# Performance work log

Hardware: AMD Instinct MI355X
Metric: run time of the kernel (lower is better)

The kernel has to match this reference:

```python
import jax, jax.numpy as jnp
import numpy as np

B, NX, NY, H = 512, 128, 128, 512


def setup_inputs() -> dict:
    key = jax.random.key(0)
    ks = jax.random.split(key, 8)
    s1 = 1.0 / np.sqrt(NX + NY)
    s2 = 1.0 / np.sqrt(H)
    return {
        "x": jax.random.normal(ks[0], (B, NX), dtype=jnp.float32),
        "y": jax.random.normal(ks[1], (B, NY), dtype=jnp.float32),
        "W1": jax.random.normal(ks[2], (H, NX + NY), dtype=jnp.float32) * s1,
        "b1": jax.random.normal(ks[3], (H,), dtype=jnp.float32) * s1,
        "W2": jax.random.normal(ks[4], (H, H), dtype=jnp.float32) * s2,
        "b2": jax.random.normal(ks[5], (H,), dtype=jnp.float32) * s2,
        "W3": jax.random.normal(ks[6], (1, H), dtype=jnp.float32) * s2,
        "b3": jax.random.normal(ks[7], (1,), dtype=jnp.float32) * s2,
    }


def reference(x, y, W1, b1, W2, b2, W3, b3):
    # Torch semantics: pair_input row k = concat(x[k % B], y[k // B]),
    # so scores.view(B,B)[i, j] = mlp(concat(x[j], y[i])).
    Nx = x.shape[1]
    hx = jnp.einsum('jn,hn->jh', x, W1[:, :Nx])          # [B_x, H]
    hy = jnp.einsum('in,hn->ih', y, W1[:, Nx:])          # [B_y, H]
    h1 = jax.nn.relu(hy[:, None, :] + hx[None, :, :] + b1)   # [B_y, B_x, H]
    h2 = jax.nn.relu(jnp.einsum('ijh,gh->ijg', h1, W2) + b2)  # [B_y, B_x, H]
    scores = jnp.einsum('ijh,oh->ijo', h2, W3) + b3          # [B_y, B_x, 1]
    return (scores[..., 0], 0.0)
```

## Files before the change

### kernel.cpp

```cpp
#include <hip/hip_runtime.h>

#define B_ 512
#define H_ 512

typedef short short8 __attribute__((ext_vector_type(8)));
typedef float f32x4 __attribute__((ext_vector_type(4)));

__device__ __forceinline__ unsigned short bf16rne(float f) {
  unsigned u = __float_as_uint(f);
  u += 0x7FFFu + ((u >> 16) & 1u);
  return (unsigned short)(u >> 16);
}

__global__ __launch_bounds__(256) void k_pre(const float* __restrict__ x,
                                             const float* __restrict__ y,
                                             const float* __restrict__ W1,
                                             const float* __restrict__ b1,
                                             const float* __restrict__ W2,
                                             float* __restrict__ hx,
                                             float* __restrict__ hy,
                                             unsigned short* __restrict__ w2p) {
  __shared__ float xs[4][128];
  const int blk = blockIdx.x;
  const int t = threadIdx.x;
  if (blk < 256) {
    const bool isx = blk < 128;
    const int r0 = (isx ? blk : blk - 128) * 4;
    const float* src = (isx ? x : y) + r0 * 128;
    if (t < 128) ((float4*)xs)[t] = ((const float4*)src)[t];
    __syncthreads();
    const int woff = isx ? 0 : 128;
    float* dst = (isx ? hx : hy) + r0 * H_;
#pragma unroll
    for (int hh = 0; hh < 2; ++hh) {
      const int h = t + hh * 256;
      const float4* wr = (const float4*)(W1 + h * 256 + woff);
      float a0 = isx ? b1[h] : 0.f, a1 = a0, a2 = a0, a3 = a0;
#pragma unroll
      for (int n = 0; n < 32; ++n) {
        float4 w = wr[n];
        float4 v0 = ((const float4*)xs[0])[n];
        float4 v1 = ((const float4*)xs[1])[n];
        float4 v2 = ((const float4*)xs[2])[n];
        float4 v3 = ((const float4*)xs[3])[n];
        a0 = fmaf(w.x, v0.x, fmaf(w.y, v0.y, fmaf(w.z, v0.z, fmaf(w.w, v0.w, a0))));
        a1 = fmaf(w.x, v1.x, fmaf(w.y, v1.y, fmaf(w.z, v1.z, fmaf(w.w, v1.w, a1))));
        a2 = fmaf(w.x, v2.x, fmaf(w.y, v2.y, fmaf(w.z, v2.z, fmaf(w.w, v2.w, a2))));
        a3 = fmaf(w.x, v3.x, fmaf(w.y, v3.y, fmaf(w.z, v3.z, fmaf(w.w, v3.w, a3))));
      }
      dst[h] = a0;
      dst[H_ + h] = a1;
      dst[2 * H_ + h] = a2;
      dst[3 * H_ + h] = a3;
    }
  } else {
    int d = (blk - 256) * 256 + t;
    int e = d & 7;
    int g15 = (d >> 3) & 15;
    int ks = (d >> 7) & 3;
    int nf = (d >> 9) & 7;
    int plane = (d >> 12) & 1;
    int c = (d >> 13) & 15;
    int nt = (d >> 17) & 3;
    int g = nt * 128 + nf * 16 + g15;
    int k = c * 32 + ks * 8 + e;
    float v = W2[g * H_ + k];
    unsigned short h = bf16rne(v);
    float r = v - __uint_as_float(((unsigned)h) << 16);
    w2p[d] = plane ? bf16rne(r) : h;
  }
}

__device__ __forceinline__ unsigned chop2(float x0, float x1, float y0,
                                          float y1) {
  float t0 = fmaxf(x0 + y0, 0.f);
  float t1 = fmaxf(x1 + y1, 0.f);
  return __builtin_amdgcn_perm(__float_as_uint(t1), __float_as_uint(t0),
                               0x07060302);
}

union Frag { unsigned u[4]; short8 s; };

#define BUILD_FRAG(NXT, m_)                                                   \
  {                                                                           \
    NXT[m_].u[0] = chop2(X0.x, X0.y, Ya[m_].x, Ya[m_].y);                     \
    NXT[m_].u[1] = chop2(X0.z, X0.w, Ya[m_].z, Ya[m_].w);                     \
    NXT[m_].u[2] = chop2(X1.x, X1.y, Yb[m_].x, Yb[m_].y);                     \
    NXT[m_].u[3] = chop2(X1.z, X1.w, Yb[m_].z, Yb[m_].w);                     \
  }

#define CHUNK_STEP(c_, buf_, CUR, NXT)                                        \
  {                                                                           \
    if ((c_) < 15) STAGE((c_) + 1, (buf_) ^ 1);                               \
    const int ko_ = ((c_) + 1) * 32;                                          \
    X0 = *(const float4*)(hxp + ko_);                                         \
    X1 = *(const float4*)(hxp + ko_ + 4);                                     \
    _Pragma("unroll") for (int m = 0; m < 4; ++m) {                           \
      Ya[m] = *(const float4*)(hyp + m * H_ + ko_);                           \
      Yb[m] = *(const float4*)(hyp + m * H_ + ko_ + 4);                       \
    }                                                                         \
    const unsigned short* bb_ = (buf_) ? bbr1 : bbr0;                         \
    _Pragma("unroll") for (int nf = 0; nf < 8; ++nf) {                        \
      short8 Bh = *(const short8*)(bb_ + nf * 512);                           \
      short8 Bl = *(const short8*)(bb_ + 4096 + nf * 512);                    \
      __builtin_amdgcn_s_setprio(1);                                          \
      _Pragma("unroll") for (int m = 0; m < 4; ++m) {                         \
        f32x4 a = acc[m][nf];                                                 \
        a = __builtin_amdgcn_mfma_f32_16x16x32_bf16(CUR[m].s, Bl, a, 0, 0, 0);\
        a = __builtin_amdgcn_mfma_f32_16x16x32_bf16(CUR[m].s, Bh, a, 0, 0, 0);\
        acc[m][nf] = a;                                                       \
      }                                                                       \
      __builtin_amdgcn_s_setprio(0);                                          \
      if ((nf) >= 4) BUILD_FRAG(NXT, (nf) - 4);                               \
    }                                                                         \
    __syncthreads();                                                          \
  }

__global__ __launch_bounds__(256, 2) void k_main(
    const float* __restrict__ hx, const float* __restrict__ hy,
    const unsigned short* __restrict__ w2p,
    const float* __restrict__ b2, const float* __restrict__ w3,
    const float* __restrict__ b3, float* __restrict__ out) {
  __shared__ alignas(16) unsigned short Bs[2][8192];

  const int tid = threadIdx.x;
  const int lane = tid & 63;
  const int wid = tid >> 6;

  const int bid = blockIdx.x;
  const int ntile = bid & 3;
  const int mtile = bid >> 2;
  const int ibase = (mtile >> 5) << 4;
  const int jbase = (mtile & 31) << 4;
  const int l15 = lane & 15;
  const int kslot = (lane >> 4) << 3;

  const float* hxp = hx + (jbase + l15) * H_ + kslot;
  const float* hyp = hy + (ibase + wid * 4) * H_ + kslot;

  const unsigned short* gstage = w2p + ntile * 131072 + wid * 2048 + lane * 8;
  unsigned short* lds_dst0 = &Bs[0][wid * 2048];
  unsigned short* lds_dst1 = &Bs[1][wid * 2048];
  const unsigned short* bbr0 = &Bs[0][0] + lane * 8;
  const unsigned short* bbr1 = &Bs[1][0] + lane * 8;

  auto STAGE = [&](int c, int buf) {
    const unsigned short* g = gstage + c * 8192;
    unsigned short* l = buf ? lds_dst1 : lds_dst0;
#pragma unroll
    for (int q = 0; q < 4; ++q) {
      __builtin_amdgcn_global_load_lds(
          (const __attribute__((address_space(1))) unsigned int*)(g + q * 512),
          (__attribute__((address_space(3))) unsigned int*)(l + q * 512),
          16, 0, 0);
    }
  };

  f32x4 acc[4][8] = {};
  Frag F[4], G[4];
  float4 X0, X1, Ya[4], Yb[4];

  STAGE(0, 0);
  X0 = *(const float4*)(hxp);
  X1 = *(const float4*)(hxp + 4);
#pragma unroll
  for (int m = 0; m < 4; ++m) {
    Ya[m] = *(const float4*)(hyp + m * H_);
    Yb[m] = *(const float4*)(hyp + m * H_ + 4);
  }
#pragma unroll
  for (int m = 0; m < 4; ++m) BUILD_FRAG(F, m);
  __syncthreads();

  for (int cc = 0; cc < 8; ++cc) {
    CHUNK_STEP(2 * cc, 0, F, G);
    CHUNK_STEP(2 * cc + 1, 1, G, F);
  }

  const int gbase = ntile << 7;
  float b2v[8], w3v[8];
#pragma unroll
  for (int nf = 0; nf < 8; ++nf) {
    int g = gbase + nf * 16 + l15;
    b2v[nf] = b2[g];
    w3v[nf] = w3[g];
  }
  const float b3v = (ntile == 0) ? b3[0] : 0.f;
#pragma unroll
  for (int mf = 0; mf < 4; ++mf) {
#pragma unroll
    for (int r = 0; r < 4; ++r) {
      float s = 0.f;
#pragma unroll
      for (int nf = 0; nf < 8; ++nf) {
        float h2 = fmaxf(acc[mf][nf][r] + b2v[nf], 0.f);
        s = fmaf(w3v[nf], h2, s);
      }
      s += __shfl_xor(s, 1);
      s += __shfl_xor(s, 2);
      s += __shfl_xor(s, 4);
      s += __shfl_xor(s, 8);
      if (l15 == 0) {
        int jl = ((lane >> 4) << 2) + r;
        int il = wid * 4 + mf;
        atomicAdd(out + (ibase + il) * B_ + jbase + jl, s + b3v);
      }
    }
  }
}

extern "C" void kernel_launch(void* const* d_in, const int* in_sizes, int n_in,
                              void* d_out, int out_size, void* d_ws, size_t ws_size,
                              hipStream_t stream) {
  const float* x  = (const float*)d_in[0];
  const float* y  = (const float*)d_in[1];
  const float* W1 = (const float*)d_in[2];
  const float* b1 = (const float*)d_in[3];
  const float* W2 = (const float*)d_in[4];
  const float* b2 = (const float*)d_in[5];
  const float* W3 = (const float*)d_in[6];
  const float* b3 = (const float*)d_in[7];
  float* out = (float*)d_out;

  char* ws = (char*)d_ws;
  float* hx = (float*)ws;
  float* hy = (float*)(ws + (1u << 20));
  unsigned short* w2p = (unsigned short*)(ws + (2u << 20));

  hipMemsetAsync(d_out, 0, (size_t)out_size * sizeof(float), stream);
  k_pre<<<2304, 256, 0, stream>>>(x, y, W1, b1, W2, hx, hy, w2p);
  k_main<<<4096, 256, 0, stream>>>(hx, hy, w2p, b2, W3, b3, out);
}
```

Baseline: 302.6 us.

## Stage two W2 chunks per barrier with doubled LDS and split lo/hi MFMA passes

Doubles the LDS staging buffer so each pipeline step prefetches two K-chunks of W2 at once. This halves the number of __syncthreads barriers in the main loop and also reorders the MFMAs into separate Bl and Bh passes. LDS use per block doubles to 64KB, which could threaten the two-blocks-per-CU occupancy. The loop is also pinned to no unrolling.

After: 314.8 us. 4.0% more time.

```diff
diff --git a/kernel.cpp b/kernel.cpp
--- a/kernel.cpp
+++ b/kernel.cpp
@@ -89,9 +89,8 @@
     NXT[m_].u[3] = chop2(X1.z, X1.w, Yb[m_].z, Yb[m_].w);                     \
   }
 
-#define CHUNK_STEP(c_, buf_, CUR, NXT)                                        \
+#define CHUNK_BODY(c_, bank_, half_, CUR, NXT)                                \
   {                                                                           \
-    if ((c_) < 15) STAGE((c_) + 1, (buf_) ^ 1);                               \
     const int ko_ = ((c_) + 1) * 32;                                          \
     X0 = *(const float4*)(hxp + ko_);                                         \
     X1 = *(const float4*)(hxp + ko_ + 4);                                     \
@@ -99,21 +98,28 @@
       Ya[m] = *(const float4*)(hyp + m * H_ + ko_);                           \
       Yb[m] = *(const float4*)(hyp + m * H_ + ko_ + 4);                       \
     }                                                                         \
-    const unsigned short* bb_ = (buf_) ? bbr1 : bbr0;                         \
+    const unsigned short* bb_ = &Bs[bank_][half_][0] + lane * 8;              \
     _Pragma("unroll") for (int nf = 0; nf < 8; ++nf) {                        \
-      short8 Bh = *(const short8*)(bb_ + nf * 512);                           \
       short8 Bl = *(const short8*)(bb_ + 4096 + nf * 512);                    \
       __builtin_amdgcn_s_setprio(1);                                          \
       _Pragma("unroll") for (int m = 0; m < 4; ++m) {                         \
-        f32x4 a = acc[m][nf];                                                 \
-        a = __builtin_amdgcn_mfma_f32_16x16x32_bf16(CUR[m].s, Bl, a, 0, 0, 0);\
-        a = __builtin_amdgcn_mfma_f32_16x16x32_bf16(CUR[m].s, Bh, a, 0, 0, 0);\
-        acc[m][nf] = a;                                                       \
+        acc[m][nf] =                                                          \
+            __builtin_amdgcn_mfma_f32_16x16x32_bf16(CUR[m].s, Bl, acc[m][nf], \
+                                                    0, 0, 0);                 \
+      }                                                                       \
+      __builtin_amdgcn_s_setprio(0);                                          \
+    }                                                                         \
+    _Pragma("unroll") for (int nf = 0; nf < 8; ++nf) {                        \
+      short8 Bh = *(const short8*)(bb_ + nf * 512);                           \
+      __builtin_amdgcn_s_setprio(1);                                          \
+      _Pragma("unroll") for (int m = 0; m < 4; ++m) {                         \
+        acc[m][nf] =                                                          \
+            __builtin_amdgcn_mfma_f32_16x16x32_bf16(CUR[m].s, Bh, acc[m][nf], \
+                                                    0, 0, 0);                 \
       }                                                                       \
       __builtin_amdgcn_s_setprio(0);                                          \
       if ((nf) >= 4) BUILD_FRAG(NXT, (nf) - 4);                               \
     }                                                                         \
-    __syncthreads();                                                          \
   }
 
 __global__ __launch_bounds__(256, 2) void k_main(
@@ -121,7 +127,7 @@
     const unsigned short* __restrict__ w2p,
     const float* __restrict__ b2, const float* __restrict__ w3,
     const float* __restrict__ b3, float* __restrict__ out) {
-  __shared__ alignas(16) unsigned short Bs[2][8192];
+  __shared__ alignas(16) unsigned short Bs[2][2][8192];
 
   const int tid = threadIdx.x;
   const int lane = tid & 63;
@@ -139,20 +145,19 @@
   const float* hyp = hy + (ibase + wid * 4) * H_ + kslot;
 
   const unsigned short* gstage = w2p + ntile * 131072 + wid * 2048 + lane * 8;
-  unsigned short* lds_dst0 = &Bs[0][wid * 2048];
-  unsigned short* lds_dst1 = &Bs[1][wid * 2048];
-  const unsigned short* bbr0 = &Bs[0][0] + lane * 8;
-  const unsigned short* bbr1 = &Bs[1][0] + lane * 8;
-
-  auto STAGE = [&](int c, int buf) {
-    const unsigned short* g = gstage + c * 8192;
-    unsigned short* l = buf ? lds_dst1 : lds_dst0;
-#pragma unroll
-    for (int q = 0; q < 4; ++q) {
-      __builtin_amdgcn_global_load_lds(
-          (const __attribute__((address_space(1))) unsigned int*)(g + q * 512),
-          (__attribute__((address_space(3))) unsigned int*)(l + q * 512),
-          16, 0, 0);
+
+  auto STAGE2 = [&](int p, int bank) {
+#pragma unroll
+    for (int h = 0; h < 2; ++h) {
+      const unsigned short* g = gstage + (2 * p + h) * 8192;
+      unsigned short* l = &Bs[bank][h][wid * 2048];
+#pragma unroll
+      for (int q = 0; q < 4; ++q) {
+        __builtin_amdgcn_global_load_lds(
+            (const __attribute__((address_space(1))) unsigned int*)(g + q * 512),
+            (__attribute__((address_space(3))) unsigned int*)(l + q * 512),
+            16, 0, 0);
+      }
     }
   };
 
@@ -160,7 +165,7 @@
   Frag F[4], G[4];
   float4 X0, X1, Ya[4], Yb[4];
 
-  STAGE(0, 0);
+  STAGE2(0, 0);
   X0 = *(const float4*)(hxp);
   X1 = *(const float4*)(hxp + 4);
 #pragma unroll
@@ -172,9 +177,13 @@
   for (int m = 0; m < 4; ++m) BUILD_FRAG(F, m);
   __syncthreads();
 
-  for (int cc = 0; cc < 8; ++cc) {
-    CHUNK_STEP(2 * cc, 0, F, G);
-    CHUNK_STEP(2 * cc + 1, 1, G, F);
+#pragma unroll 1
+  for (int p = 0; p < 8; ++p) {
+    const int bank = p & 1;
+    if (p < 7) STAGE2(p + 1, bank ^ 1);
+    CHUNK_BODY(2 * p, bank, 0, F, G);
+    CHUNK_BODY(2 * p + 1, bank, 1, G, F);
+    __syncthreads();
   }
 
   const int gbase = ntile << 7;
```
